# Kernel tuning notes

Hardware: AMD Instinct MI355X
Metric: run time of the kernel (lower is better)

The kernel has to match this reference:

```python
import jax, jax.numpy as jnp
import numpy as np

SEQ = 8192
DIM = 1024

def setup_inputs() -> dict:
    key = jax.random.key(0)
    kx, kq, kk, kv1, kv2 = jax.random.split(key, 5)
    std = 0.01  # flax nn.initializers.normal() default stddev=1e-2
    return {
        "x": jax.random.normal(kx, (SEQ, DIM), dtype=jnp.float32),
        "wq": jax.random.normal(kq, (DIM, DIM), dtype=jnp.float32) * std,
        "wk": jax.random.normal(kk, (DIM, DIM), dtype=jnp.float32) * std,
        "wv1": jax.random.normal(kv1, (DIM, DIM), dtype=jnp.float32) * std,
        "wv2": jax.random.normal(kv2, (DIM, DIM), dtype=jnp.float32) * std,
    }

def reference(x, wq, wk, wv1, wv2):
    # x: [S, D]; single-head causal self-attention with SiLU-gated output proj
    q = x @ wq              # [S, D]
    k = x @ wk              # [S, D]
    v = x @ wv1             # [S, D]
    dim_head = q.shape[-1]
    dots = (q @ k.T) * (dim_head ** -0.5)          # [S, S]
    s = x.shape[-2]
    mask = jnp.tril(jnp.ones((s, s), dtype=bool))
    dots = jnp.where(mask, dots, -1e9)
    attn = jax.nn.softmax(dots, axis=-1)            # [S, S]
    hidden = attn @ v                               # [S, D]
    return jax.nn.silu(hidden) @ wv2                # [S, D]
```

## Files before the change

### kernel.cpp

```cpp
#include <hip/hip_runtime.h>
#include <hip/hip_bf16.h>
#include <cstdint>
#include <cstddef>

constexpr int SEQ = 8192;
constexpr int DIM = 1024;

typedef __attribute__((ext_vector_type(8))) short short8;
typedef __attribute__((ext_vector_type(4))) float f32x4;
typedef __attribute__((ext_vector_type(4))) unsigned short us4;

#define MFMA_BF16 __builtin_amdgcn_mfma_f32_16x16x32_bf16

static __device__ __forceinline__ unsigned short f2bf(float f) {
    uint32_t u = __builtin_bit_cast(uint32_t, f);
    u += 0x7FFFu + ((u >> 16) & 1u);
    return (unsigned short)(u >> 16);
}
static __device__ __forceinline__ float bf2f(unsigned short h) {
    uint32_t u = ((uint32_t)h) << 16;
    return __builtin_bit_cast(float, u);
}
static __device__ __forceinline__ int r64(int x) {
    return ((x + 32) >> 6) << 6;
}

#define GLOAD16(gp, lp) __builtin_amdgcn_global_load_lds(                      \
    (const __attribute__((address_space(1))) void*)(gp),                       \
    (__attribute__((address_space(3))) void*)(lp), 16, 0, 0)

template<int OM, bool CAUSAL, bool KCAP, bool SILU, bool SPLITK>
__global__ __launch_bounds__(256, 4)
void gemm_bt(const unsigned short* __restrict__ A,
             const unsigned short* __restrict__ Bt,
             void* __restrict__ Cp,
             int M, int N, int K, float scale, int rowBase, int NS)
{
    constexpr int BM = 128, BK = 64, BN = 128;
    constexpr int NF = BN / 32;
    __shared__ __align__(16) unsigned short As[BM * BK];
    __shared__ __align__(16) unsigned short Bs[BN * BK];

    const int t = threadIdx.x;
    const int lane = t & 63, w = t >> 6;
    const int wr = w >> 1, wc = w & 1;
    const int ln15 = lane & 15, hi = lane >> 4;

    const int gx = gridDim.x, gy = gridDim.y;
    const int nwg = gx * gy * gridDim.z;
    const int orig = blockIdx.y + gy * (blockIdx.x + gx * blockIdx.z);
    const int q = nwg >> 3, r8 = nwg & 7;
    const int xcd = orig & 7, idx = orig >> 3;
    const int wg = (xcd < r8 ? xcd * (q + 1)
                             : r8 * (q + 1) + (xcd - r8) * q) + idx;
    const int byi = wg % gy, tmpw = wg / gy;
    const int bxi = tmpw % gx, bzi = tmpw / gx;

    const int bm = byi * BM, bn = bxi * BN;

    if (CAUSAL && bn > rowBase + bm + (BM - 1)) return;
    int Keff = K;
    if (KCAP) { int kc = rowBase + bm + BM; Keff = kc < K ? kc : K; }
    int kbeg = 0, kend = Keff;
    if (SPLITK) {
        kbeg = r64(bzi * Keff / NS);
        int ke = r64((bzi + 1) * Keff / NS);
        kend = ke < Keff ? ke : Keff;
        if (kbeg >= kend) return;
    }

    f32x4 acc[4][NF] = {};

    for (int k0 = kbeg; k0 < kend; k0 += BK) {
        #pragma unroll
        for (int i = 0; i < 4; ++i) {
            int c = t + 256 * i;
            int r = c >> 3, qq = (c & 7) ^ (r & 7);
            GLOAD16(A + (size_t)(bm + r) * K + k0 + qq * 8, As + c * 8);
        }
        #pragma unroll
        for (int i = 0; i < 4; ++i) {
            int c = t + 256 * i;
            int r = c >> 3, qq = (c & 7) ^ (r & 7);
            GLOAD16(Bt + (size_t)(bn + r) * K + k0 + qq * 8, Bs + c * 8);
        }
        __syncthreads();

        #pragma unroll
        for (int kk = 0; kk < 2; ++kk) {
            short8 a[4], b[NF];
            #pragma unroll
            for (int m = 0; m < 4; ++m) {
                int r = wr * 64 + m * 16 + ln15;
                int s = (kk * 4 + hi) ^ (r & 7);
                a[m] = *(const short8*)(As + r * 64 + s * 8);
            }
            #pragma unroll
            for (int n = 0; n < NF; ++n) {
                int r = wc * 64 + n * 16 + ln15;
                int s = (kk * 4 + hi) ^ (r & 7);
                b[n] = *(const short8*)(Bs + r * 64 + s * 8);
            }
            __builtin_amdgcn_s_setprio(1);
            #pragma unroll
            for (int m = 0; m < 4; ++m)
                #pragma unroll
                for (int n = 0; n < NF; ++n)
                    acc[m][n] = MFMA_BF16(a[m], b[n], acc[m][n], 0, 0, 0);
            __builtin_amdgcn_s_setprio(0);
        }
        __syncthreads();
    }

    float* Pz = (OM == 3)
        ? (float*)Cp + (size_t)bzi * M * N : nullptr;
    #pragma unroll
    for (int m = 0; m < 4; ++m)
        #pragma unroll
        for (int n = 0; n < NF; ++n)
            #pragma unroll
            for (int j = 0; j < 4; ++j) {
                int row = bm + wr * 64 + m * 16 + hi * 4 + j;
                int col = bn + wc * 64 + n * 16 + ln15;
                float v = acc[m][n][j] * scale;
                if (SILU) v = v / (1.0f + __expf(-v));
                if (OM == 0)
                    ((unsigned short*)Cp)[(size_t)row * N + col] = f2bf(v);
                else if (OM == 1)
                    ((unsigned short*)Cp)[(size_t)col * M + row] = f2bf(v);
                else if (OM == 2)
                    ((float*)Cp)[(size_t)row * N + col] = v;
                else
                    Pz[(size_t)row * N + col] = v;
            }
}

__global__ __launch_bounds__(256)
void reduce_silu(const float* __restrict__ part, unsigned short* __restrict__ out,
                 int ns, int rowBase)
{
    const size_t idx = ((size_t)blockIdx.x * 256 + threadIdx.x) * 8;
    const int r = (int)(idx >> 10);
    int keb = rowBase + ((r >> 7) << 7) + 128;
    if (keb > SEQ) keb = SEQ;

    f32x4 s0 = {}, s1 = {};
    for (int z = 0; z < ns; ++z) {
        int b0 = r64(z * keb / ns);
        int b1 = r64((z + 1) * keb / ns);
        if (b1 > keb) b1 = keb;
        if (b1 > b0) {
            const float* p = part + (size_t)z * (2048 * 1024) + idx;
            s0 += *(const f32x4*)p;
            s1 += *(const f32x4*)(p + 4);
        }
    }
    short8 o;
    #pragma unroll
    for (int j = 0; j < 4; ++j) {
        float v = s0[j];
        o[j] = (short)f2bf(v / (1.0f + __expf(-v)));
    }
    #pragma unroll
    for (int j = 0; j < 4; ++j) {
        float v = s1[j];
        o[4 + j] = (short)f2bf(v / (1.0f + __expf(-v)));
    }
    *(short8*)(out + idx) = o;
}

__global__ __launch_bounds__(256)
void softmax_rows(unsigned short* __restrict__ S, int rowBase)
{
    __shared__ float red[4];
    const int r = blockIdx.x;
    const int grow = rowBase + r;
    const int Kcap = ((grow >> 7) + 1) << 7;
    unsigned short* row = S + (size_t)r * SEQ;
    const int t = threadIdx.x, lane = t & 63, w = t >> 6;

    float v[4][8];
    float mx = -1e30f;
    #pragma unroll
    for (int i = 0; i < 4; ++i) {
        int c0 = (i * 256 + t) * 8;
        if (c0 < Kcap) {
            short8 s8 = *(const short8*)(row + c0);
            #pragma unroll
            for (int j = 0; j < 8; ++j) {
                float f = bf2f((unsigned short)s8[j]);
                v[i][j] = (c0 + j <= grow) ? f : -1e30f;
                mx = fmaxf(mx, v[i][j]);
            }
        } else {
            #pragma unroll
            for (int j = 0; j < 8; ++j) v[i][j] = -1e30f;
        }
    }
    #pragma unroll
    for (int off = 32; off >= 1; off >>= 1)
        mx = fmaxf(mx, __shfl_xor(mx, off, 64));
    if (lane == 0) red[w] = mx;
    __syncthreads();
    mx = fmaxf(fmaxf(red[0], red[1]), fmaxf(red[2], red[3]));
    __syncthreads();

    float sum = 0.f;
    #pragma unroll
    for (int i = 0; i < 4; ++i)
        #pragma unroll
        for (int j = 0; j < 8; ++j) {
            float p = (v[i][j] > -1e29f) ? __expf(v[i][j] - mx) : 0.f;
            v[i][j] = p;
            sum += p;
        }
    #pragma unroll
    for (int off = 32; off >= 1; off >>= 1)
        sum += __shfl_xor(sum, off, 64);
    if (lane == 0) red[w] = sum;
    __syncthreads();
    sum = red[0] + red[1] + red[2] + red[3];
    const float inv = 1.0f / sum;

    #pragma unroll
    for (int i = 0; i < 4; ++i) {
        int c0 = (i * 256 + t) * 8;
        if (c0 < Kcap) {
            short8 o;
            #pragma unroll
            for (int j = 0; j < 8; ++j) o[j] = (short)f2bf(v[i][j] * inv);
            *(short8*)(row + c0) = o;
        }
    }
}

__global__ __launch_bounds__(256)
void cvt_bf16(const float* __restrict__ X, unsigned short* __restrict__ Y)
{
    int i = (blockIdx.x * 256 + threadIdx.x) * 8;
    f32x4 v0 = *(const f32x4*)(X + i);
    f32x4 v1 = *(const f32x4*)(X + i + 4);
    short8 o = { (short)f2bf(v0[0]), (short)f2bf(v0[1]),
                 (short)f2bf(v0[2]), (short)f2bf(v0[3]),
                 (short)f2bf(v1[0]), (short)f2bf(v1[1]),
                 (short)f2bf(v1[2]), (short)f2bf(v1[3]) };
    *(short8*)(Y + i) = o;
}

__global__ __launch_bounds__(256)
void twT(const float* __restrict__ W, unsigned short* __restrict__ WT)
{
    __shared__ float tile[64][65];
    const int bx = blockIdx.x * 64, by = blockIdx.y * 64;
    const int t = threadIdx.x, rr = t >> 4, c4 = (t & 15) * 4;
    #pragma unroll
    for (int i = 0; i < 4; ++i) {
        int r = rr + i * 16;
        f32x4 v = *(const f32x4*)(W + (size_t)(by + r) * DIM + bx + c4);
        tile[r][c4 + 0] = v[0]; tile[r][c4 + 1] = v[1];
        tile[r][c4 + 2] = v[2]; tile[r][c4 + 3] = v[3];
    }
    __syncthreads();
    #pragma unroll
    for (int i = 0; i < 4; ++i) {
        int r = rr + i * 16;
        us4 o = { f2bf(tile[c4 + 0][r]), f2bf(tile[c4 + 1][r]),
                  f2bf(tile[c4 + 2][r]), f2bf(tile[c4 + 3][r]) };
        *(us4*)(WT + (size_t)(bx + r) * DIM + by + c4) = o;
    }
}

extern "C" void kernel_launch(void* const* d_in, const int* in_sizes, int n_in,
                              void* d_out, int out_size, void* d_ws, size_t ws_size,
                              hipStream_t stream)
{
    const float* x   = (const float*)d_in[0];
    const float* wq  = (const float*)d_in[1];
    const float* wk  = (const float*)d_in[2];
    const float* wv1 = (const float*)d_in[3];
    const float* wv2 = (const float*)d_in[4];

    const size_t BUF = (size_t)SEQ * DIM * sizeof(unsigned short);
    unsigned short* qbuf  = (unsigned short*)d_ws;
    unsigned short* kbuf  = qbuf + (size_t)SEQ * DIM;
    unsigned short* vtbuf = kbuf + (size_t)SEQ * DIM;
    float* part = (float*)((char*)d_ws + 3 * BUF);
    const size_t PSZ = (size_t)2048 * 1024 * sizeof(float);
    int nsplit = 0;
    if (ws_size >= 3 * BUF + 2 * PSZ) {
        size_t ns = (ws_size - 3 * BUF) / PSZ;
        nsplit = (int)(ns < 4 ? ns : 4);
    }

    unsigned short* xb    = (unsigned short*)d_out;
    unsigned short* wqT   = xb + (size_t)SEQ * DIM;
    unsigned short* wkT   = wqT + DIM * DIM;
    unsigned short* wv1T  = wkT + DIM * DIM;
    unsigned short* Sband = (unsigned short*)d_out;

    dim3 tg(16, 16);
    cvt_bf16<<<SEQ * DIM / 2048, 256, 0, stream>>>(x, xb);
    twT<<<tg, 256, 0, stream>>>(wq,  wqT);
    twT<<<tg, 256, 0, stream>>>(wk,  wkT);
    twT<<<tg, 256, 0, stream>>>(wv1, wv1T);

    dim3 gproj(DIM / 128, SEQ / 128);
    gemm_bt<0,false,false,false,false><<<gproj, 256, 0, stream>>>(
        xb, wqT,  qbuf,  SEQ, DIM, DIM, 1.0f, 0, 0);
    gemm_bt<0,false,false,false,false><<<gproj, 256, 0, stream>>>(
        xb, wkT,  kbuf,  SEQ, DIM, DIM, 1.0f, 0, 0);
    gemm_bt<1,false,false,false,false><<<gproj, 256, 0, stream>>>(
        xb, wv1T, vtbuf, SEQ, DIM, DIM, 1.0f, 0, 0);

    constexpr int BAND = 2048;
    for (int b = 0; b < 4; ++b) {
        const int rb = b * BAND;
        const int ncol = (rb + BAND) / 128;
        dim3 gq(ncol, BAND / 128);
        gemm_bt<0,true,false,false,false><<<gq, 256, 0, stream>>>(
            qbuf + (size_t)rb * DIM, kbuf, Sband, BAND, SEQ, DIM, 0.03125f, rb, 0);
        if (b == 3)
            twT<<<tg, 256, 0, stream>>>(wv2, kbuf);
        softmax_rows<<<BAND, 256, 0, stream>>>(Sband, rb);
        if (nsplit >= 2) {
            dim3 gpv(DIM / 128, BAND / 128, nsplit);
            gemm_bt<3,false,true,false,true><<<gpv, 256, 0, stream>>>(
                Sband, vtbuf, part, BAND, DIM, SEQ, 1.0f, rb, nsplit);
            reduce_silu<<<BAND * DIM / 2048, 256, 0, stream>>>(
                part, qbuf + (size_t)rb * DIM, nsplit, rb);
        } else {
            dim3 gpv(DIM / 128, BAND / 128);
            gemm_bt<0,false,true,true,false><<<gpv, 256, 0, stream>>>(
                Sband, vtbuf, qbuf + (size_t)rb * DIM, BAND, DIM, SEQ, 1.0f, rb, 0);
        }
    }

    gemm_bt<2,false,false,false,false><<<gproj, 256, 0, stream>>>(
        qbuf, kbuf, d_out, SEQ, DIM, DIM, 1.0f, 0, 0);
}
```

Measured before the change: 387.4 us.

## Fuse QKV projection and process full attention matrix in single launches

Merges the three projection GEMMs into one launch over a concatenated transposed weight, routing output columns to Q, K and transposed V. Replaces the four-band loop with one full-size score GEMM, one softmax and one split-K PV GEMM over the whole sequence, holding the full SxS bf16 score matrix in workspace. Split-K partials are now bf16 instead of fp32 with a fixed split count of 4, which halves partial traffic but loses accumulation precision. It needs a much larger workspace and no longer checks ws_size, and the causal score GEMM grid launches all tiles, relying on in-kernel skipping of tiles above the diagonal.

```diff
diff --git a/kernel.cpp b/kernel.cpp
--- a/kernel.cpp
+++ b/kernel.cpp
@@ -29,7 +29,7 @@
     (const __attribute__((address_space(1))) void*)(gp),                       \
     (__attribute__((address_space(3))) void*)(lp), 16, 0, 0)
 
-template<int OM, bool CAUSAL, bool KCAP, bool SILU, bool SPLITK>
+template<int OM, bool CAUSAL, bool KCAP, bool SPLITK>
 __global__ __launch_bounds__(256, 4)
 void gemm_bt(const unsigned short* __restrict__ A,
              const unsigned short* __restrict__ Bt,
@@ -112,8 +112,6 @@
         __syncthreads();
     }
 
-    float* Pz = (OM == 3)
-        ? (float*)Cp + (size_t)bzi * M * N : nullptr;
     #pragma unroll
     for (int m = 0; m < 4; ++m)
         #pragma unroll
@@ -123,59 +121,62 @@
                 int row = bm + wr * 64 + m * 16 + hi * 4 + j;
                 int col = bn + wc * 64 + n * 16 + ln15;
                 float v = acc[m][n][j] * scale;
-                if (SILU) v = v / (1.0f + __expf(-v));
                 if (OM == 0)
                     ((unsigned short*)Cp)[(size_t)row * N + col] = f2bf(v);
-                else if (OM == 1)
-                    ((unsigned short*)Cp)[(size_t)col * M + row] = f2bf(v);
                 else if (OM == 2)
                     ((float*)Cp)[(size_t)row * N + col] = v;
-                else
-                    Pz[(size_t)row * N + col] = v;
+                else if (OM == 3)
+                    ((unsigned short*)Cp + (size_t)bzi * M * N)
+                        [(size_t)row * N + col] = f2bf(v);
+                else {
+                    unsigned short* qb = (unsigned short*)Cp;
+                    if (col < DIM)
+                        qb[(size_t)row * DIM + col] = f2bf(v);
+                    else if (col < 2 * DIM)
+                        (qb + (size_t)SEQ * DIM)
+                            [(size_t)row * DIM + (col - DIM)] = f2bf(v);
+                    else
+                        (qb + (size_t)2 * SEQ * DIM)
+                            [(size_t)(col - 2 * DIM) * SEQ + row] = f2bf(v);
+                }
             }
 }
 
 __global__ __launch_bounds__(256)
-void reduce_silu(const float* __restrict__ part, unsigned short* __restrict__ out,
-                 int ns, int rowBase)
+void reduce_silu(const unsigned short* __restrict__ part,
+                 unsigned short* __restrict__ out, int ns)
 {
     const size_t idx = ((size_t)blockIdx.x * 256 + threadIdx.x) * 8;
     const int r = (int)(idx >> 10);
-    int keb = rowBase + ((r >> 7) << 7) + 128;
+    int keb = ((r >> 7) << 7) + 128;
     if (keb > SEQ) keb = SEQ;
 
-    f32x4 s0 = {}, s1 = {};
+    float s[8] = {};
     for (int z = 0; z < ns; ++z) {
         int b0 = r64(z * keb / ns);
         int b1 = r64((z + 1) * keb / ns);
         if (b1 > keb) b1 = keb;
         if (b1 > b0) {
-            const float* p = part + (size_t)z * (2048 * 1024) + idx;
-            s0 += *(const f32x4*)p;
-            s1 += *(const f32x4*)(p + 4);
+            short8 p = *(const short8*)(part + (size_t)z * SEQ * DIM + idx);
+            #pragma unroll
+            for (int j = 0; j < 8; ++j) s[j] += bf2f((unsigned short)p[j]);
         }
     }
     short8 o;
     #pragma unroll
-    for (int j = 0; j < 4; ++j) {
-        float v = s0[j];
+    for (int j = 0; j < 8; ++j) {
+        float v = s[j];
         o[j] = (short)f2bf(v / (1.0f + __expf(-v)));
     }
-    #pragma unroll
-    for (int j = 0; j < 4; ++j) {
-        float v = s1[j];
-        o[4 + j] = (short)f2bf(v / (1.0f + __expf(-v)));
-    }
     *(short8*)(out + idx) = o;
 }
 
 __global__ __launch_bounds__(256)
-void softmax_rows(unsigned short* __restrict__ S, int rowBase)
+void softmax_rows(unsigned short* __restrict__ S)
 {
     __shared__ float red[4];
     const int r = blockIdx.x;
-    const int grow = rowBase + r;
-    const int Kcap = ((grow >> 7) + 1) << 7;
+    const int Kcap = ((r >> 7) + 1) << 7;
     unsigned short* row = S + (size_t)r * SEQ;
     const int t = threadIdx.x, lane = t & 63, w = t >> 6;
 
@@ -189,7 +190,7 @@
             #pragma unroll
             for (int j = 0; j < 8; ++j) {
                 float f = bf2f((unsigned short)s8[j]);
-                v[i][j] = (c0 + j <= grow) ? f : -1e30f;
+                v[i][j] = (c0 + j <= r) ? f : -1e30f;
                 mx = fmaxf(mx, v[i][j]);
             }
         } else {
@@ -280,61 +281,37 @@
     const float* wv1 = (const float*)d_in[3];
     const float* wv2 = (const float*)d_in[4];
 
-    const size_t BUF = (size_t)SEQ * DIM * sizeof(unsigned short);
+    const size_t E = (size_t)SEQ * DIM;
     unsigned short* qbuf  = (unsigned short*)d_ws;
-    unsigned short* kbuf  = qbuf + (size_t)SEQ * DIM;
-    unsigned short* vtbuf = kbuf + (size_t)SEQ * DIM;
-    float* part = (float*)((char*)d_ws + 3 * BUF);
-    const size_t PSZ = (size_t)2048 * 1024 * sizeof(float);
-    int nsplit = 0;
-    if (ws_size >= 3 * BUF + 2 * PSZ) {
-        size_t ns = (ws_size - 3 * BUF) / PSZ;
-        nsplit = (int)(ns < 4 ? ns : 4);
-    }
-
-    unsigned short* xb    = (unsigned short*)d_out;
-    unsigned short* wqT   = xb + (size_t)SEQ * DIM;
-    unsigned short* wkT   = wqT + DIM * DIM;
-    unsigned short* wv1T  = wkT + DIM * DIM;
-    unsigned short* Sband = (unsigned short*)d_out;
+    unsigned short* kbuf  = qbuf + E;
+    unsigned short* vtbuf = kbuf + E;
+    unsigned short* Sfull = vtbuf + E;
+    unsigned short* part  = Sfull + (size_t)SEQ * SEQ;
+
+    unsigned short* xb   = (unsigned short*)d_out;
+    unsigned short* wqkv = xb + E;
+    constexpr int NS = 4;
 
     dim3 tg(16, 16);
     cvt_bf16<<<SEQ * DIM / 2048, 256, 0, stream>>>(x, xb);
-    twT<<<tg, 256, 0, stream>>>(wq,  wqT);
-    twT<<<tg, 256, 0, stream>>>(wk,  wkT);
-    twT<<<tg, 256, 0, stream>>>(wv1, wv1T);
-
-    dim3 gproj(DIM / 128, SEQ / 128);
-    gemm_bt<0,false,false,false,false><<<gproj, 256, 0, stream>>>(
-        xb, wqT,  qbuf,  SEQ, DIM, DIM, 1.0f, 0, 0);
-    gemm_bt<0,false,false,false,false><<<gproj, 256, 0, stream>>>(
-        xb, wkT,  kbuf,  SEQ, DIM, DIM, 1.0f, 0, 0);
-    gemm_bt<1,false,false,false,false><<<gproj, 256, 0, stream>>>(
-        xb, wv1T, vtbuf, SEQ, DIM, DIM, 1.0f, 0, 0);
-
-    constexpr int BAND = 2048;
-    for (int b = 0; b < 4; ++b) {
-        const int rb = b * BAND;
-        const int ncol = (rb + BAND) / 128;
-        dim3 gq(ncol, BAND / 128);
-        gemm_bt<0,true,false,false,false><<<gq, 256, 0, stream>>>(
-            qbuf + (size_t)rb * DIM, kbuf, Sband, BAND, SEQ, DIM, 0.03125f, rb, 0);
-        if (b == 3)
-            twT<<<tg, 256, 0, stream>>>(wv2, kbuf);
-        softmax_rows<<<BAND, 256, 0, stream>>>(Sband, rb);
-        if (nsplit >= 2) {
-            dim3 gpv(DIM / 128, BAND / 128, nsplit);
-            gemm_bt<3,false,true,false,true><<<gpv, 256, 0, stream>>>(
-                Sband, vtbuf, part, BAND, DIM, SEQ, 1.0f, rb, nsplit);
-            reduce_silu<<<BAND * DIM / 2048, 256, 0, stream>>>(
-                part, qbuf + (size_t)rb * DIM, nsplit, rb);
-        } else {
-            dim3 gpv(DIM / 128, BAND / 128);
-            gemm_bt<0,false,true,true,false><<<gpv, 256, 0, stream>>>(
-                Sband, vtbuf, qbuf + (size_t)rb * DIM, BAND, DIM, SEQ, 1.0f, rb, 0);
-        }
-    }
-
-    gemm_bt<2,false,false,false,false><<<gproj, 256, 0, stream>>>(
+    twT<<<tg, 256, 0, stream>>>(wq,  wqkv);
+    twT<<<tg, 256, 0, stream>>>(wk,  wqkv + DIM * DIM);
+    twT<<<tg, 256, 0, stream>>>(wv1, wqkv + 2 * DIM * DIM);
+
+    gemm_bt<4,false,false,false><<<dim3(3 * DIM / 128, SEQ / 128), 256, 0, stream>>>(
+        xb, wqkv, qbuf, SEQ, 3 * DIM, DIM, 1.0f, 0, 0);
+
+    gemm_bt<0,true,false,false><<<dim3(SEQ / 128, SEQ / 128), 256, 0, stream>>>(
+        qbuf, kbuf, Sfull, SEQ, SEQ, DIM, 0.03125f, 0, 0);
+
+    twT<<<tg, 256, 0, stream>>>(wv2, kbuf);
+
+    softmax_rows<<<SEQ, 256, 0, stream>>>(Sfull);
+
+    gemm_bt<3,false,true,true><<<dim3(DIM / 128, SEQ / 128, NS), 256, 0, stream>>>(
+        Sfull, vtbuf, part, SEQ, DIM, SEQ, 1.0f, 0, NS);
+    reduce_silu<<<SEQ * DIM / 2048, 256, 0, stream>>>(part, qbuf, NS);
+
+    gemm_bt<2,false,false,false><<<dim3(DIM / 128, SEQ / 128), 256, 0, stream>>>(
         qbuf, kbuf, d_out, SEQ, DIM, DIM, 1.0f, 0, 0);
 }
```

After: 443.7 us. 14.5% more time.
